# Kernel optimization log

Hardware: AMD Instinct MI355X
Metric: run time of the kernel (lower is better)

## Reference

```python
import jax, jax.numpy as jnp
import numpy as np

B, P, T, V, N, D = 16, 96, 128, 64, 16, 128


def setup_inputs() -> dict:
    key = jax.random.key(0)
    ks = jax.random.split(key, 9)
    s = 0.05  # weight scale for stability
    return {
        "queries": jax.random.normal(ks[0], (B, P, V, D), jnp.float32),
        "keys": jax.random.normal(ks[1], (B, T, V, D), jnp.float32),
        "var_ccc": jax.random.randint(ks[2], (B, V, N), 0, V),
        "Wq": jax.random.normal(ks[3], (D, D), jnp.float32) * s,
        "bq": jnp.zeros((D,), jnp.float32),
        "Wkv": jax.random.normal(ks[4], (D, D), jnp.float32) * s,
        "bkv": jnp.zeros((D,), jnp.float32),
        "Wout": jax.random.normal(ks[5], (D, D), jnp.float32) * s,
        "bout": jnp.zeros((D,), jnp.float32),
    }


def reference(queries, keys, var_ccc, Wq, bq, Wkv, bkv, Wout, bout):
    b, p, v, d = queries.shape
    scale = d ** -0.5
    # projections (nn.Linear: x @ W.T + b)
    q = queries @ Wq.T + bq                      # [B,P,V,D]
    k = keys @ Wkv.T + bkv                       # [B,T,V,D]
    k_last = k[:, -p:]                           # [B,P,V,D]
    # irregular gather of neighbor keys per (batch, variable)
    idx = var_ccc.reshape(b, -1)                 # [B, V*N]
    kc = jax.vmap(lambda kb, ib: kb[:, ib])(k_last, idx)  # [B,P,V*N,D]
    kc = kc.reshape(b, p, v, -1, d)              # [B,P,V,N,D] (keys == values)
    # tiny 1xN attention per (b,p,v)
    scores = jnp.einsum('bpvd,bpvnd->bpvn', q, kc) * scale
    attn = jax.nn.softmax(scores, axis=-1)       # dropout is identity in eval
    out = jnp.einsum('bpvn,bpvnd->bpvd', attn, kc)  # [B,P,V,D]
    res = jnp.concatenate([k[:, :-p], out], axis=1)  # [B,T,V,D]
    return res @ Wout.T + bout
```

## Files before the change

### kernel.cpp

```cpp
#include <hip/hip_runtime.h>

#define BB 16
#define PP 96
#define TT 128
#define VV 64
#define NN 16
#define DD 128
#define SB 136
#define ST 72

typedef __bf16 bf16x8 __attribute__((ext_vector_type(8)));
typedef __bf16 bf16x4 __attribute__((ext_vector_type(4)));
typedef float  floatx4 __attribute__((ext_vector_type(4)));

#define MFMA16(a, b, c) __builtin_amdgcn_mfma_f32_16x16x32_bf16(a, b, c, 0, 0, 0)

__global__ void combine_w(const float* __restrict__ Wout,
                          const float* __restrict__ Wkv,
                          const float* __restrict__ bkv,
                          const float* __restrict__ bout,
                          float* __restrict__ Wcomb,
                          float* __restrict__ bcomb) {
    int i = blockIdx.x, j = threadIdx.x;
    float acc = 0.f;
    for (int k = 0; k < DD; ++k) acc += Wout[i * DD + k] * Wkv[k * DD + j];
    Wcomb[i * DD + j] = acc;
    if (i == 0) {
        float b = bout[j];
        for (int k = 0; k < DD; ++k) b += Wout[j * DD + k] * bkv[k];
        bcomb[j] = b;
    }
}

__global__ void cvt_weights(const float* __restrict__ Wq,
                            const float* __restrict__ Wkv,
                            const float* __restrict__ Wout,
                            const float* __restrict__ Wcomb,
                            __bf16* __restrict__ o) {
    int i = blockIdx.x * 256 + threadIdx.x;
    o[i]             = (__bf16)Wq[i];
    o[16384 + i]     = (__bf16)Wkv[i];
    o[32768 + i]     = (__bf16)Wout[i];
    o[49152 + i]     = (__bf16)Wcomb[i];
}

__device__ __forceinline__ void mm128(const __bf16* As, int sa,
                                      const __bf16* Bm, int sb,
                                      int w, int lm, int lq,
                                      floatx4* acc, int nblocks) {
    bf16x8 af[4];
#pragma unroll
    for (int ks = 0; ks < 4; ++ks)
        af[ks] = *(const bf16x8*)(As + (w * 16 + lm) * sa + lq * 8 + 32 * ks);
#pragma unroll
    for (int nb = 0; nb < 8; ++nb) {
        if (nb >= nblocks) break;
        acc[nb] = floatx4{0.f, 0.f, 0.f, 0.f};
#pragma unroll
        for (int ks = 0; ks < 4; ++ks) {
            bf16x8 bf = *(const bf16x8*)(Bm + (nb * 16 + lm) * sb + lq * 8 + 32 * ks);
            acc[nb] = MFMA16(af[ks], bf, acc[nb]);
        }
    }
}

__global__ __launch_bounds__(256, 4) void gemm_pass(
    const float* __restrict__ X, const __bf16* __restrict__ Wc,
    const float* __restrict__ bias, float* __restrict__ Y) {
    __shared__ __align__(16) __bf16 smX[64 * SB];
    int bl = blockIdx.x;
    int b = bl >> 5, wi = bl & 31;
    const float* Xb = X + ((long)b * TT * VV + wi * 64) * DD;
    float* Yb = Y + ((long)b * TT * VV + wi * 64) * DD;
    int t = threadIdx.x, w = t >> 6, L = t & 63, lm = L & 15, lq = L >> 4;

    {
        int r = t >> 2, c0 = (t & 3) * 32;
        const float4* s4 = (const float4*)(Xb + r * DD + c0);
#pragma unroll
        for (int i = 0; i < 8; ++i) {
            float4 v = s4[i];
            *(bf16x4*)(smX + r * SB + c0 + i * 4) =
                bf16x4{(__bf16)v.x, (__bf16)v.y, (__bf16)v.z, (__bf16)v.w};
        }
    }
    __syncthreads();

    floatx4 acc[8];
    mm128(smX, SB, Wc, DD, w, lm, lq, acc, 8);
#pragma unroll
    for (int nb = 0; nb < 8; ++nb) {
        float bv = bias[nb * 16 + lm];
#pragma unroll
        for (int r = 0; r < 4; ++r)
            Yb[(long)(w * 16 + lq * 4 + r) * DD + nb * 16 + lm] = acc[nb][r] + bv;
    }
}

__global__ __launch_bounds__(256, 2) void attn_kernel(
    const float* __restrict__ queries, const float* __restrict__ keys,
    const int* __restrict__ ccc, const __bf16* __restrict__ Wb,
    const float* __restrict__ bq, const float* __restrict__ bkv,
    const float* __restrict__ bout, float* __restrict__ out) {
    __shared__ __align__(16) char lds[79872];
    __bf16* smKin = (__bf16*)lds;
    __bf16* smQin = (__bf16*)(lds + 17408);
    __bf16* smKs  = (__bf16*)(lds + 34816);
    __bf16* smKsT = (__bf16*)(lds + 52224);
    __bf16* smA   = (__bf16*)(lds + 70656);
    float*  smS   = (float*)lds;
    __bf16* smO   = smQin;

    const __bf16* Wq_b   = Wb;
    const __bf16* Wkv_b  = Wb + 16384;
    const __bf16* Wout_b = Wb + 32768;

    int bl = blockIdx.x;
    int b = bl / PP, p = bl % PP;
    int t = threadIdx.x, w = t >> 6, L = t & 63, lm = L & 15, lq = L >> 4;

    const float* Kg = keys + ((long)(b * TT + 32 + p) * VV) * DD;
    const float* Qg = queries + ((long)(b * PP + p) * VV) * DD;
    float* Yg = out + ((long)(b * TT + 32 + p) * VV) * DD;

    {
        int r = t >> 2, c0 = (t & 3) * 32;
        const float4* k4 = (const float4*)(Kg + r * DD + c0);
        const float4* q4 = (const float4*)(Qg + r * DD + c0);
#pragma unroll
        for (int i = 0; i < 8; ++i) {
            float4 kv = k4[i], qv = q4[i];
            *(bf16x4*)(smKin + r * SB + c0 + i * 4) =
                bf16x4{(__bf16)kv.x, (__bf16)kv.y, (__bf16)kv.z, (__bf16)kv.w};
            *(bf16x4*)(smQin + r * SB + c0 + i * 4) =
                bf16x4{(__bf16)qv.x, (__bf16)qv.y, (__bf16)qv.z, (__bf16)qv.w};
        }
        for (int i = t; i < VV * ST / 2; i += 256) ((unsigned int*)smA)[i] = 0u;
    }
    __syncthreads();

    floatx4 acc[8];

    mm128(smQin, SB, Wq_b, DD, w, lm, lq, acc, 8);
    __syncthreads();
#pragma unroll
    for (int nb = 0; nb < 8; ++nb) {
        float bv = bq[nb * 16 + lm];
#pragma unroll
        for (int r = 0; r < 4; ++r)
            smQin[(w * 16 + lq * 4 + r) * SB + nb * 16 + lm] = (__bf16)(acc[nb][r] + bv);
    }

    mm128(smKin, SB, Wkv_b, DD, w, lm, lq, acc, 8);
#pragma unroll
    for (int nb = 0; nb < 8; ++nb) {
        float bv = bkv[nb * 16 + lm];
        bf16x4 tp;
#pragma unroll
        for (int r = 0; r < 4; ++r) {
            float vv = acc[nb][r] + bv;
            smKs[(w * 16 + lq * 4 + r) * SB + nb * 16 + lm] = (__bf16)vv;
            tp[r] = (__bf16)vv;
        }
        *(bf16x4*)(smKsT + (nb * 16 + lm) * ST + w * 16 + lq * 4) = tp;
    }
    __syncthreads();

    mm128(smQin, SB, smKs, SB, w, lm, lq, acc, 4);
#pragma unroll
    for (int nb = 0; nb < 4; ++nb)
#pragma unroll
        for (int r = 0; r < 4; ++r)
            smS[(w * 16 + lq * 4 + r) * 68 + nb * 16 + lm] = acc[nb][r];
    __syncthreads();

    if (t < VV) {
        const int4* cp = (const int4*)(ccc + (b * VV + t) * NN);
        int se[NN];
#pragma unroll
        for (int i = 0; i < 4; ++i) {
            int4 c4 = cp[i];
            se[4 * i] = c4.x; se[4 * i + 1] = c4.y; se[4 * i + 2] = c4.z; se[4 * i + 3] = c4.w;
        }
        float sc[NN], mx = -1e30f;
#pragma unroll
        for (int n = 0; n < NN; ++n) {
            sc[n] = smS[t * 68 + se[n]] * 0.08838834764831845f;
            mx = fmaxf(mx, sc[n]);
        }
        float sum = 0.f;
#pragma unroll
        for (int n = 0; n < NN; ++n) { sc[n] = __expf(sc[n] - mx); sum += sc[n]; }
        float inv = 1.f / sum;
#pragma unroll
        for (int n = 0; n < NN; ++n) {
            int u = se[n];
            float cur = (float)smA[t * ST + u];
            smA[t * ST + u] = (__bf16)(cur + sc[n] * inv);
        }
    }
    __syncthreads();

    {
        floatx4 accO[8];
        bf16x8 af2[2];
#pragma unroll
        for (int ks = 0; ks < 2; ++ks)
            af2[ks] = *(const bf16x8*)(smA + (w * 16 + lm) * ST + lq * 8 + 32 * ks);
#pragma unroll
        for (int nb = 0; nb < 8; ++nb) {
            accO[nb] = floatx4{0.f, 0.f, 0.f, 0.f};
#pragma unroll
            for (int ks = 0; ks < 2; ++ks) {
                bf16x8 bfr = *(const bf16x8*)(smKsT + (nb * 16 + lm) * ST + lq * 8 + 32 * ks);
                accO[nb] = MFMA16(af2[ks], bfr, accO[nb]);
            }
        }
#pragma unroll
        for (int nb = 0; nb < 8; ++nb)
#pragma unroll
            for (int r = 0; r < 4; ++r)
                smO[(w * 16 + lq * 4 + r) * SB + nb * 16 + lm] = (__bf16)accO[nb][r];
    }

    mm128(smO, SB, Wout_b, DD, w, lm, lq, acc, 8);
#pragma unroll
    for (int nb = 0; nb < 8; ++nb) {
        float bv = bout[nb * 16 + lm];
#pragma unroll
        for (int r = 0; r < 4; ++r)
            Yg[(long)(w * 16 + lq * 4 + r) * DD + nb * 16 + lm] = acc[nb][r] + bv;
    }
}

extern "C" void kernel_launch(void* const* d_in, const int* in_sizes, int n_in,
                              void* d_out, int out_size, void* d_ws, size_t ws_size,
                              hipStream_t stream) {
    const float* queries = (const float*)d_in[0];
    const float* keys    = (const float*)d_in[1];
    const int*   ccc     = (const int*)d_in[2];
    const float* Wq      = (const float*)d_in[3];
    const float* bq      = (const float*)d_in[4];
    const float* Wkv     = (const float*)d_in[5];
    const float* bkv     = (const float*)d_in[6];
    const float* Wout    = (const float*)d_in[7];
    const float* bout    = (const float*)d_in[8];
    float* out = (float*)d_out;

    float*  Wcomb = (float*)d_ws;
    float*  bcomb = Wcomb + DD * DD;
    __bf16* Wb    = (__bf16*)((char*)d_ws + 66048);

    combine_w<<<dim3(128), dim3(128), 0, stream>>>(Wout, Wkv, bkv, bout, Wcomb, bcomb);
    cvt_weights<<<dim3(64), dim3(256), 0, stream>>>(Wq, Wkv, Wout, Wcomb, Wb);

    gemm_pass<<<dim3(BB * 32), dim3(256), 0, stream>>>(keys, Wb + 49152, bcomb, out);

    attn_kernel<<<dim3(BB * PP), dim3(256), 0, stream>>>(
        queries, keys, ccc, Wb, bq, bkv, bout, out);
}
```

Baseline: 262.2 us.

## Fuse weight prep and pass-through GEMM into attention kernel, load A from global

```diff
diff --git a/kernel.cpp b/kernel.cpp
--- a/kernel.cpp
+++ b/kernel.cpp
@@ -6,8 +6,11 @@
 #define VV 64
 #define NN 16
 #define DD 128
+#define BPP (BB * PP)
+#define NPASS (BB * 32)
 #define SB 136
 #define ST 72
+#define SSF 68
 
 typedef __bf16 bf16x8 __attribute__((ext_vector_type(8)));
 typedef __bf16 bf16x4 __attribute__((ext_vector_type(4)));
@@ -15,143 +18,123 @@
 
 #define MFMA16(a, b, c) __builtin_amdgcn_mfma_f32_16x16x32_bf16(a, b, c, 0, 0, 0)
 
-__global__ void combine_w(const float* __restrict__ Wout,
-                          const float* __restrict__ Wkv,
-                          const float* __restrict__ bkv,
-                          const float* __restrict__ bout,
-                          float* __restrict__ Wcomb,
-                          float* __restrict__ bcomb) {
+__device__ __forceinline__ bf16x8 cvt8(float4 a, float4 b) {
+    return bf16x8{(__bf16)a.x, (__bf16)a.y, (__bf16)a.z, (__bf16)a.w,
+                  (__bf16)b.x, (__bf16)b.y, (__bf16)b.z, (__bf16)b.w};
+}
+
+__device__ __forceinline__ void loadA_g(const float* Xs, int lm, int lq, bf16x8 af[4]) {
+    const float4* p = (const float4*)(Xs + lm * DD + lq * 8);
+#pragma unroll
+    for (int ks = 0; ks < 4; ++ks) af[ks] = cvt8(p[8 * ks], p[8 * ks + 1]);
+}
+
+__device__ __forceinline__ void loadA_l(const __bf16* As, int sa, int lm, int lq,
+                                        bf16x8* af, int kblocks) {
+#pragma unroll
+    for (int ks = 0; ks < 4; ++ks) {
+        if (ks >= kblocks) break;
+        af[ks] = *(const bf16x8*)(As + lm * sa + lq * 8 + 32 * ks);
+    }
+}
+
+__device__ __forceinline__ void mmB(const bf16x8* af, const __bf16* B, int sb,
+                                    int lm, int lq, floatx4* acc, int nblocks, int kblocks) {
+#pragma unroll
+    for (int nb = 0; nb < 8; ++nb) {
+        if (nb >= nblocks) break;
+        acc[nb] = floatx4{0.f, 0.f, 0.f, 0.f};
+#pragma unroll
+        for (int ks = 0; ks < 4; ++ks) {
+            if (ks >= kblocks) break;
+            bf16x8 bf = *(const bf16x8*)(B + (nb * 16 + lm) * sb + lq * 8 + 32 * ks);
+            acc[nb] = MFMA16(af[ks], bf, acc[nb]);
+        }
+    }
+}
+
+__global__ void prep(const float* __restrict__ Wq, const float* __restrict__ Wkv,
+                     const float* __restrict__ Wout, const float* __restrict__ bkv,
+                     const float* __restrict__ bout,
+                     __bf16* __restrict__ Wb, float* __restrict__ bcomb) {
     int i = blockIdx.x, j = threadIdx.x;
+    Wb[i * DD + j]         = (__bf16)Wq[i * DD + j];
+    Wb[16384 + i * DD + j] = (__bf16)Wkv[i * DD + j];
+    Wb[32768 + i * DD + j] = (__bf16)Wout[i * DD + j];
     float acc = 0.f;
     for (int k = 0; k < DD; ++k) acc += Wout[i * DD + k] * Wkv[k * DD + j];
-    Wcomb[i * DD + j] = acc;
+    Wb[49152 + i * DD + j] = (__bf16)acc;
     if (i == 0) {
-        float b = bout[j];
-        for (int k = 0; k < DD; ++k) b += Wout[j * DD + k] * bkv[k];
-        bcomb[j] = b;
-    }
-}
-
-__global__ void cvt_weights(const float* __restrict__ Wq,
-                            const float* __restrict__ Wkv,
-                            const float* __restrict__ Wout,
-                            const float* __restrict__ Wcomb,
-                            __bf16* __restrict__ o) {
-    int i = blockIdx.x * 256 + threadIdx.x;
-    o[i]             = (__bf16)Wq[i];
-    o[16384 + i]     = (__bf16)Wkv[i];
-    o[32768 + i]     = (__bf16)Wout[i];
-    o[49152 + i]     = (__bf16)Wcomb[i];
-}
-
-__device__ __forceinline__ void mm128(const __bf16* As, int sa,
-                                      const __bf16* Bm, int sb,
-                                      int w, int lm, int lq,
-                                      floatx4* acc, int nblocks) {
-    bf16x8 af[4];
-#pragma unroll
-    for (int ks = 0; ks < 4; ++ks)
-        af[ks] = *(const bf16x8*)(As + (w * 16 + lm) * sa + lq * 8 + 32 * ks);
-#pragma unroll
-    for (int nb = 0; nb < 8; ++nb) {
-        if (nb >= nblocks) break;
-        acc[nb] = floatx4{0.f, 0.f, 0.f, 0.f};
-#pragma unroll
-        for (int ks = 0; ks < 4; ++ks) {
-            bf16x8 bf = *(const bf16x8*)(Bm + (nb * 16 + lm) * sb + lq * 8 + 32 * ks);
-            acc[nb] = MFMA16(af[ks], bf, acc[nb]);
-        }
-    }
-}
-
-__global__ __launch_bounds__(256, 4) void gemm_pass(
-    const float* __restrict__ X, const __bf16* __restrict__ Wc,
-    const float* __restrict__ bias, float* __restrict__ Y) {
-    __shared__ __align__(16) __bf16 smX[64 * SB];
-    int bl = blockIdx.x;
-    int b = bl >> 5, wi = bl & 31;
-    const float* Xb = X + ((long)b * TT * VV + wi * 64) * DD;
-    float* Yb = Y + ((long)b * TT * VV + wi * 64) * DD;
-    int t = threadIdx.x, w = t >> 6, L = t & 63, lm = L & 15, lq = L >> 4;
-
-    {
-        int r = t >> 2, c0 = (t & 3) * 32;
-        const float4* s4 = (const float4*)(Xb + r * DD + c0);
-#pragma unroll
-        for (int i = 0; i < 8; ++i) {
-            float4 v = s4[i];
-            *(bf16x4*)(smX + r * SB + c0 + i * 4) =
-                bf16x4{(__bf16)v.x, (__bf16)v.y, (__bf16)v.z, (__bf16)v.w};
-        }
-    }
-    __syncthreads();
-
-    floatx4 acc[8];
-    mm128(smX, SB, Wc, DD, w, lm, lq, acc, 8);
-#pragma unroll
-    for (int nb = 0; nb < 8; ++nb) {
-        float bv = bias[nb * 16 + lm];
-#pragma unroll
-        for (int r = 0; r < 4; ++r)
-            Yb[(long)(w * 16 + lq * 4 + r) * DD + nb * 16 + lm] = acc[nb][r] + bv;
-    }
-}
-
-__global__ __launch_bounds__(256, 2) void attn_kernel(
+        float bs = bout[j];
+        for (int k = 0; k < DD; ++k) bs += Wout[j * DD + k] * bkv[k];
+        bcomb[j] = bs;
+    }
+}
+
+__global__ __launch_bounds__(256, 3) void fused(
     const float* __restrict__ queries, const float* __restrict__ keys,
     const int* __restrict__ ccc, const __bf16* __restrict__ Wb,
     const float* __restrict__ bq, const float* __restrict__ bkv,
-    const float* __restrict__ bout, float* __restrict__ out) {
-    __shared__ __align__(16) char lds[79872];
-    __bf16* smKin = (__bf16*)lds;
-    __bf16* smQin = (__bf16*)(lds + 17408);
-    __bf16* smKs  = (__bf16*)(lds + 34816);
-    __bf16* smKsT = (__bf16*)(lds + 52224);
-    __bf16* smA   = (__bf16*)(lds + 70656);
+    const float* __restrict__ bout, const float* __restrict__ bcomb,
+    float* __restrict__ out) {
+    __shared__ __align__(16) char lds[53248];
+    __bf16* R1    = (__bf16*)lds;
+    __bf16* smKs  = (__bf16*)(lds + 17408);
+    __bf16* smKsT = (__bf16*)(lds + 34816);
+    __bf16* smA   = smKs;
     float*  smS   = (float*)lds;
-    __bf16* smO   = smQin;
-
-    const __bf16* Wq_b   = Wb;
-    const __bf16* Wkv_b  = Wb + 16384;
-    const __bf16* Wout_b = Wb + 32768;
-
-    int bl = blockIdx.x;
+
+    int bl = blockIdx.x, t = threadIdx.x;
+    int w = t >> 6, L = t & 63, lm = L & 15, lq = L >> 4;
+
+    bf16x8 af[4];
+    floatx4 acc[8];
+
+    if (bl >= BPP) {
+        int pb = bl - BPP;
+        int b = pb >> 5, wi = pb & 31;
+        const float* Xs = keys + ((long)b * TT * VV + wi * 64 + w * 16) * DD;
+        float* Yg = out + ((long)b * TT * VV + wi * 64) * DD;
+        loadA_g(Xs, lm, lq, af);
+        mmB(af, Wb + 49152, DD, lm, lq, acc, 8, 4);
+#pragma unroll
+        for (int nb = 0; nb < 8; ++nb) {
+            float bv = bcomb[nb * 16 + lm];
+#pragma unroll
+            for (int r = 0; r < 4; ++r)
+                Yg[(long)(w * 16 + lq * 4 + r) * DD + nb * 16 + lm] = acc[nb][r] + bv;
+        }
+        return;
+    }
+
     int b = bl / PP, p = bl % PP;
-    int t = threadIdx.x, w = t >> 6, L = t & 63, lm = L & 15, lq = L >> 4;
-
+    const float* Qg = queries + ((long)(b * PP + p) * VV) * DD;
     const float* Kg = keys + ((long)(b * TT + 32 + p) * VV) * DD;
-    const float* Qg = queries + ((long)(b * PP + p) * VV) * DD;
     float* Yg = out + ((long)(b * TT + 32 + p) * VV) * DD;
 
-    {
-        int r = t >> 2, c0 = (t & 3) * 32;
-        const float4* k4 = (const float4*)(Kg + r * DD + c0);
-        const float4* q4 = (const float4*)(Qg + r * DD + c0);
-#pragma unroll
-        for (int i = 0; i < 8; ++i) {
-            float4 kv = k4[i], qv = q4[i];
-            *(bf16x4*)(smKin + r * SB + c0 + i * 4) =
-                bf16x4{(__bf16)kv.x, (__bf16)kv.y, (__bf16)kv.z, (__bf16)kv.w};
-            *(bf16x4*)(smQin + r * SB + c0 + i * 4) =
-                bf16x4{(__bf16)qv.x, (__bf16)qv.y, (__bf16)qv.z, (__bf16)qv.w};
-        }
-        for (int i = t; i < VV * ST / 2; i += 256) ((unsigned int*)smA)[i] = 0u;
-    }
-    __syncthreads();
-
-    floatx4 acc[8];
-
-    mm128(smQin, SB, Wq_b, DD, w, lm, lq, acc, 8);
-    __syncthreads();
+    int se[NN];
+    if (L < 16) {
+        const int4* cp = (const int4*)(ccc + ((long)b * VV + w * 16 + L) * NN);
+#pragma unroll
+        for (int i = 0; i < 4; ++i) {
+            int4 c4 = cp[i];
+            se[4 * i] = c4.x; se[4 * i + 1] = c4.y;
+            se[4 * i + 2] = c4.z; se[4 * i + 3] = c4.w;
+        }
+    }
+
+    loadA_g(Qg + w * 16 * DD, lm, lq, af);
+    mmB(af, Wb, DD, lm, lq, acc, 8, 4);
 #pragma unroll
     for (int nb = 0; nb < 8; ++nb) {
         float bv = bq[nb * 16 + lm];
 #pragma unroll
         for (int r = 0; r < 4; ++r)
-            smQin[(w * 16 + lq * 4 + r) * SB + nb * 16 + lm] = (__bf16)(acc[nb][r] + bv);
-    }
-
-    mm128(smKin, SB, Wkv_b, DD, w, lm, lq, acc, 8);
+            R1[(w * 16 + lq * 4 + r) * SB + nb * 16 + lm] = (__bf16)(acc[nb][r] + bv);
+    }
+
+    loadA_g(Kg + w * 16 * DD, lm, lq, af);
+    mmB(af, Wb + 16384, DD, lm, lq, acc, 8, 4);
 #pragma unroll
     for (int nb = 0; nb < 8; ++nb) {
         float bv = bkv[nb * 16 + lm];
@@ -166,64 +149,48 @@
     }
     __syncthreads();
 
-    mm128(smQin, SB, smKs, SB, w, lm, lq, acc, 4);
+    loadA_l(R1 + w * 16 * SB, SB, lm, lq, af, 4);
+    mmB(af, smKs, SB, lm, lq, acc, 4, 4);
 #pragma unroll
     for (int nb = 0; nb < 4; ++nb)
 #pragma unroll
         for (int r = 0; r < 4; ++r)
-            smS[(w * 16 + lq * 4 + r) * 68 + nb * 16 + lm] = acc[nb][r];
+            smS[(w * 16 + lq * 4 + r) * SSF + nb * 16 + lm] = acc[nb][r];
     __syncthreads();
 
-    if (t < VV) {
-        const int4* cp = (const int4*)(ccc + (b * VV + t) * NN);
-        int se[NN];
-#pragma unroll
-        for (int i = 0; i < 4; ++i) {
-            int4 c4 = cp[i];
-            se[4 * i] = c4.x; se[4 * i + 1] = c4.y; se[4 * i + 2] = c4.z; se[4 * i + 3] = c4.w;
-        }
-        float sc[NN], mx = -1e30f;
-#pragma unroll
-        for (int n = 0; n < NN; ++n) {
-            sc[n] = smS[t * 68 + se[n]] * 0.08838834764831845f;
-            mx = fmaxf(mx, sc[n]);
-        }
-        float sum = 0.f;
-#pragma unroll
-        for (int n = 0; n < NN; ++n) { sc[n] = __expf(sc[n] - mx); sum += sc[n]; }
-        float inv = 1.f / sum;
-#pragma unroll
-        for (int n = 0; n < NN; ++n) {
-            int u = se[n];
-            float cur = (float)smA[t * ST + u];
-            smA[t * ST + u] = (__bf16)(cur + sc[n] * inv);
-        }
-    }
-    __syncthreads();
-
     {
-        floatx4 accO[8];
-        bf16x8 af2[2];
-#pragma unroll
-        for (int ks = 0; ks < 2; ++ks)
-            af2[ks] = *(const bf16x8*)(smA + (w * 16 + lm) * ST + lq * 8 + 32 * ks);
-#pragma unroll
-        for (int nb = 0; nb < 8; ++nb) {
-            accO[nb] = floatx4{0.f, 0.f, 0.f, 0.f};
-#pragma unroll
-            for (int ks = 0; ks < 2; ++ks) {
-                bf16x8 bfr = *(const bf16x8*)(smKsT + (nb * 16 + lm) * ST + lq * 8 + 32 * ks);
-                accO[nb] = MFMA16(af2[ks], bfr, accO[nb]);
+        unsigned* za = (unsigned*)(smA + (w * 16) * ST);
+        for (int i = L; i < 16 * ST / 2; i += 64) za[i] = 0u;
+        if (L < 16) {
+            int v = w * 16 + L;
+            float sc[NN], mx = -1e30f;
+#pragma unroll
+            for (int n = 0; n < NN; ++n) {
+                sc[n] = smS[v * SSF + se[n]] * 0.08838834764831845f;
+                mx = fmaxf(mx, sc[n]);
             }
-        }
-#pragma unroll
-        for (int nb = 0; nb < 8; ++nb)
-#pragma unroll
-            for (int r = 0; r < 4; ++r)
-                smO[(w * 16 + lq * 4 + r) * SB + nb * 16 + lm] = (__bf16)accO[nb][r];
-    }
-
-    mm128(smO, SB, Wout_b, DD, w, lm, lq, acc, 8);
+            float sum = 0.f;
+#pragma unroll
+            for (int n = 0; n < NN; ++n) { sc[n] = __expf(sc[n] - mx); sum += sc[n]; }
+            float inv = 1.f / sum;
+#pragma unroll
+            for (int n = 0; n < NN; ++n) {
+                int u = se[n];
+                smA[v * ST + u] = (__bf16)((float)smA[v * ST + u] + sc[n] * inv);
+            }
+        }
+    }
+
+    loadA_l(smA + w * 16 * ST, ST, lm, lq, af, 2);
+    mmB(af, smKsT, ST, lm, lq, acc, 8, 2);
+#pragma unroll
+    for (int nb = 0; nb < 8; ++nb)
+#pragma unroll
+        for (int r = 0; r < 4; ++r)
+            R1[(w * 16 + lq * 4 + r) * SB + nb * 16 + lm] = (__bf16)acc[nb][r];
+
+    loadA_l(R1 + w * 16 * SB, SB, lm, lq, af, 4);
+    mmB(af, Wb + 32768, DD, lm, lq, acc, 8, 4);
 #pragma unroll
     for (int nb = 0; nb < 8; ++nb) {
         float bv = bout[nb * 16 + lm];
@@ -247,15 +214,11 @@
     const float* bout    = (const float*)d_in[8];
     float* out = (float*)d_out;
 
-    float*  Wcomb = (float*)d_ws;
-    float*  bcomb = Wcomb + DD * DD;
-    __bf16* Wb    = (__bf16*)((char*)d_ws + 66048);
-
-    combine_w<<<dim3(128), dim3(128), 0, stream>>>(Wout, Wkv, bkv, bout, Wcomb, bcomb);
-    cvt_weights<<<dim3(64), dim3(256), 0, stream>>>(Wq, Wkv, Wout, Wcomb, Wb);
-
-    gemm_pass<<<dim3(BB * 32), dim3(256), 0, stream>>>(keys, Wb + 49152, bcomb, out);
-
-    attn_kernel<<<dim3(BB * PP), dim3(256), 0, stream>>>(
-        queries, keys, ccc, Wb, bq, bkv, bout, out);
-}
+    __bf16* Wb    = (__bf16*)d_ws;
+    float*  bcomb = (float*)((char*)d_ws + 131072);
+
+    prep<<<dim3(128), dim3(128), 0, stream>>>(Wq, Wkv, Wout, bkv, bout, Wb, bcomb);
+
+    fused<<<dim3(BPP + NPASS), dim3(256), 0, stream>>>(
+        queries, keys, ccc, Wb, bq, bkv, bout, bcomb, out);
+}
```

Result: faster. 252.7 us (-3.6%).
